# Optimization experiments

Hardware: AMD Instinct MI355X
Metric: run time of the kernel (lower is better)

Reference implementation:

```python
import jax, jax.numpy as jnp
import numpy as np

N_NODES = 50000
N_EDGES = 800000
N_GRAPHS = 512
IN_DIM, HID_DIM, EMB_DIM = 128, 256, 128
EPS = 1e-5


def setup_inputs() -> dict:
    key = jax.random.key(0)
    ks = jax.random.split(key, 12)
    x = jax.random.normal(ks[0], (N_NODES, IN_DIM), dtype=jnp.float32)
    edge_index = jax.random.randint(ks[1], (2, N_EDGES), 0, N_NODES, dtype=jnp.int32)
    batch = jnp.sort(jax.random.randint(ks[2], (N_NODES,), 0, N_GRAPHS, dtype=jnp.int32))
    s1 = 1.0 / np.sqrt(IN_DIM)
    s2 = 1.0 / np.sqrt(HID_DIM)
    return {
        "x": x,
        "edge_index": edge_index,
        "batch": batch,
        "W1": jax.random.uniform(ks[3], (IN_DIM, HID_DIM), jnp.float32, -s1, s1),
        "b1": jnp.zeros((HID_DIM,), jnp.float32),
        "gamma1": jnp.ones((HID_DIM,), jnp.float32),
        "beta1": jnp.zeros((HID_DIM,), jnp.float32),
        "W2": jax.random.uniform(ks[4], (HID_DIM, EMB_DIM), jnp.float32, -s2, s2),
        "b2": jnp.zeros((EMB_DIM,), jnp.float32),
        "gamma2": jnp.ones((EMB_DIM,), jnp.float32),
        "beta2": jnp.zeros((EMB_DIM,), jnp.float32),
    }


def _gcn_conv(x, W, b, src, dst, n_nodes):
    # PyG GCNConv: h = xW; aggregate with sym-normalized adjacency incl. self-loops; + bias
    h = x @ W  # [N, D]
    ones = jnp.ones(src.shape[0], dtype=h.dtype)
    deg = jax.ops.segment_sum(ones, dst, num_segments=n_nodes) + 1.0  # self-loop
    dinv = jax.lax.rsqrt(deg)
    norm = dinv[src] * dinv[dst]  # [E]
    msg = h[src] * norm[:, None]  # gather + scale  [E, D]
    agg = jax.ops.segment_sum(msg, dst, num_segments=n_nodes)
    agg = agg + h * (1.0 / deg)[:, None]  # self-loop contribution (norm = 1/deg)
    return agg + b


def _batchnorm(h, gamma, beta):
    mean = jnp.mean(h, axis=0)
    var = jnp.mean(jnp.square(h - mean), axis=0)  # biased, training mode
    return gamma * (h - mean) * jax.lax.rsqrt(var + EPS) + beta


def reference(x, edge_index, batch, W1, b1, gamma1, beta1, W2, b2, gamma2, beta2):
    src, dst = edge_index[0], edge_index[1]
    n = x.shape[0]
    h = _gcn_conv(x, W1, b1, src, dst, n)
    h = _batchnorm(jax.nn.relu(h), gamma1, beta1)
    h = _gcn_conv(h, W2, b2, src, dst, n)
    h = _batchnorm(jax.nn.relu(h), gamma2, beta2)
    return jax.ops.segment_max(h, batch, num_segments=N_GRAPHS)
```

## Files before the change

### kernel.cpp

```cpp
#include <hip/hip_runtime.h>
#include <math.h>

#define N_NODES 50000
#define N_EDGES 800000
#define N_GRAPHS 512
#define IN_DIM 128
#define HID_DIM 256
#define EMB_DIM 128
#define EPS 1e-5f
#define ELLW 64
#define NGROUP 8
#define GROUPN 6250
#define BLK_PER_GROUP 256
#define SCAT_BLOCKS (NGROUP * BLK_PER_GROUP)
#define NV4 (N_EDGES / 4)
#define EPV4 ((NV4 + BLK_PER_GROUP - 1) / BLK_PER_GROUP)
#define F2B_N (N_NODES * IN_DIM / 4)
#define F2B_BLOCKS ((F2B_N + 255) / 256)
#define TW1_BLOCKS ((HID_DIM * IN_DIM + 255) / 256)
#define NSLOTS 128
#define GSLOTS 128

typedef __attribute__((ext_vector_type(8))) short bf16x8;
typedef __attribute__((ext_vector_type(4))) float f32x4;
typedef __attribute__((ext_vector_type(4))) int i32x4;
typedef __attribute__((ext_vector_type(4))) unsigned short u16x4;

static __device__ __forceinline__ unsigned short f2b(float f) {
    unsigned u = __float_as_uint(f);
    return (unsigned short)((u + 0x7fffu + ((u >> 16) & 1u)) >> 16);
}
static __device__ __forceinline__ float b2f(unsigned short h) {
    return __uint_as_float(((unsigned)h) << 16);
}
static __device__ __forceinline__ float dinv_of(int d) {
    return rsqrtf((float)(min(d, ELLW) + 1));
}

__global__ void __launch_bounds__(256) scatter_convert(const int* __restrict__ src,
                                                       const int* __restrict__ dst,
                                                       int* __restrict__ fill,
                                                       int* __restrict__ col,
                                                       const float* __restrict__ x,
                                                       unsigned short* __restrict__ xbf,
                                                       const float* __restrict__ W1,
                                                       unsigned short* __restrict__ W1t) {
    int b = blockIdx.x;
    if (b < SCAT_BLOCKS) {
        int g = b & 7;
        int bs = b >> 3;
        int lo = g * GROUPN;
        int hi = lo + GROUPN;
        int i_end = min((bs + 1) * EPV4, NV4);
        const i32x4* dst4 = (const i32x4*)dst;
        const i32x4* src4 = (const i32x4*)src;
        for (int i = bs * EPV4 + threadIdx.x; i < i_end; i += 256) {
            i32x4 d4 = __builtin_nontemporal_load(&dst4[i]);
            i32x4 s4 = __builtin_nontemporal_load(&src4[i]);
#pragma unroll
            for (int e = 0; e < 4; ++e) {
                int d = d4[e];
                if (d >= lo && d < hi) {
                    int pos = min(atomicAdd(&fill[d], 1), ELLW - 1);
                    col[(d << 6) + pos] = s4[e];
                }
            }
        }
    } else if (b < SCAT_BLOCKS + F2B_BLOCKS) {
        int i = (b - SCAT_BLOCKS) * 256 + threadIdx.x;
        if (i < F2B_N) {
            f32x4 v = __builtin_nontemporal_load(&((const f32x4*)x)[i]);
            u16x4 o;
            o[0] = f2b(v[0]); o[1] = f2b(v[1]); o[2] = f2b(v[2]); o[3] = f2b(v[3]);
            __builtin_nontemporal_store(o, &((u16x4*)xbf)[i]);
        }
    } else {
        int j = (b - SCAT_BLOCKS - F2B_BLOCKS) * 256 + threadIdx.x;
        if (j < HID_DIM * IN_DIM) {
            int n = j >> 7;
            int k = j & 127;
            W1t[j] = f2b(W1[k * HID_DIM + n]);
        }
    }
}

static __device__ __forceinline__ void acc8(float* acc, uint4 r, float w) {
    const unsigned* u = (const unsigned*)&r;
#pragma unroll
    for (int k = 0; k < 4; ++k) {
        float lo = __uint_as_float((u[k] & 0xFFFFu) << 16);
        float hi = __uint_as_float(u[k] & 0xFFFF0000u);
        acc[2 * k]     += w * lo;
        acc[2 * k + 1] += w * hi;
    }
}

template <bool RELU, bool OUT_BF, bool BIAS, bool STATS>
__global__ void __launch_bounds__(256) aggw_kernel(const unsigned short* __restrict__ h,
                                                   const int* __restrict__ deg,
                                                   const int* __restrict__ col,
                                                   const float* __restrict__ bias,
                                                   void* __restrict__ y,
                                                   float* __restrict__ sumP,
                                                   float* __restrict__ sqP) {
    __shared__ float sv[STATS ? 4 : 1][STATS ? 128 : 1];
    int tid = threadIdx.x;
    int lane = tid & 63;
    int wid = tid >> 6;
    int v = blockIdx.x * 4 + wid;
    int g = lane >> 4;
    int p = lane & 15;

    int dcl = min(deg[v], ELLW);
    int cv = col[(v << 6) + lane];
    int u_l = (lane < dcl) ? cv : v;
    float w_l = (lane < dcl) ? dinv_of(deg[u_l]) : 0.f;

    uint4 selfr = make_uint4(0u, 0u, 0u, 0u);
    if (g == 0) selfr = *(const uint4*)(h + (size_t)v * 128 + p * 8);

    float acc[8] = {};
    for (int base = 0; base < dcl; base += 16) {
        int i0 = base + g, i1 = base + 4 + g, i2 = base + 8 + g, i3 = base + 12 + g;
        int u0 = __shfl(u_l, i0, 64), u1 = __shfl(u_l, i1, 64);
        int u2 = __shfl(u_l, i2, 64), u3 = __shfl(u_l, i3, 64);
        float w0 = __shfl(w_l, i0, 64), w1 = __shfl(w_l, i1, 64);
        float w2 = __shfl(w_l, i2, 64), w3 = __shfl(w_l, i3, 64);
        uint4 d0 = *(const uint4*)(h + (size_t)u0 * 128 + p * 8);
        uint4 d1 = *(const uint4*)(h + (size_t)u1 * 128 + p * 8);
        uint4 d2 = *(const uint4*)(h + (size_t)u2 * 128 + p * 8);
        uint4 d3 = *(const uint4*)(h + (size_t)u3 * 128 + p * 8);
        acc8(acc, d0, w0);
        acc8(acc, d1, w1);
        acc8(acc, d2, w2);
        acc8(acc, d3, w3);
    }

#pragma unroll
    for (int k = 0; k < 8; ++k) {
        float a = acc[k];
        a += __shfl_xor(a, 16, 64);
        a += __shfl_xor(a, 32, 64);
        acc[k] = a;
    }

    if (g == 0) {
        const unsigned* su = (const unsigned*)&selfr;
        float dv = rsqrtf((float)(dcl + 1));
        float dv2 = dv * dv;
        float o[8];
#pragma unroll
        for (int k = 0; k < 4; ++k) {
            float lo = __uint_as_float((su[k] & 0xFFFFu) << 16);
            float hi = __uint_as_float(su[k] & 0xFFFF0000u);
            o[2 * k]     = dv * acc[2 * k]     + lo * dv2;
            o[2 * k + 1] = dv * acc[2 * k + 1] + hi * dv2;
        }
        if (BIAS) {
            float4 bv0 = *(const float4*)&bias[p * 8];
            float4 bv1 = *(const float4*)&bias[p * 8 + 4];
            o[0] += bv0.x; o[1] += bv0.y; o[2] += bv0.z; o[3] += bv0.w;
            o[4] += bv1.x; o[5] += bv1.y; o[6] += bv1.z; o[7] += bv1.w;
        }
        if (RELU) {
#pragma unroll
            for (int k = 0; k < 8; ++k) o[k] = fmaxf(o[k], 0.f);
        }
        if (OUT_BF) {
            uint4 packed;
            unsigned* pu = (unsigned*)&packed;
#pragma unroll
            for (int k = 0; k < 4; ++k)
                pu[k] = (unsigned)f2b(o[2 * k]) | ((unsigned)f2b(o[2 * k + 1]) << 16);
            *(uint4*)((unsigned short*)y + (size_t)v * 128 + p * 8) = packed;
        } else {
            float* yf = (float*)y + (size_t)v * 128 + p * 8;
            *(float4*)yf = make_float4(o[0], o[1], o[2], o[3]);
            *(float4*)(yf + 4) = make_float4(o[4], o[5], o[6], o[7]);
        }
        if (STATS) {
#pragma unroll
            for (int k = 0; k < 8; ++k) sv[wid][p * 8 + k] = o[k];
        }
    }

    if (STATS) {
        __syncthreads();
        if (tid < 128) {
            float s = 0.f, q = 0.f;
#pragma unroll
            for (int w = 0; w < 4; ++w) {
                float val = sv[w][tid];
                s += val;
                q += val * val;
            }
            int slot = blockIdx.x & (NSLOTS - 1);
            atomicAdd(&sumP[slot * 128 + tid], s);
            atomicAdd(&sqP[slot * 128 + tid], q);
        }
    }
}

template <bool RELU, bool STATS>
__global__ void __launch_bounds__(256) mfma_gemm_kernel(const unsigned short* __restrict__ A,
                                                        const unsigned short* __restrict__ Bt,
                                                        const float* __restrict__ bias,
                                                        unsigned short* __restrict__ C,
                                                        float* __restrict__ sums,
                                                        float* __restrict__ sumsqs,
                                                        int M, int N, int K) {
    const int LDT = 40;
    __shared__ unsigned short As[64 * LDT];
    __shared__ unsigned short Bs[64 * LDT];
    int tid = threadIdx.x;
    int bm = blockIdx.x * 64;
    int bn = blockIdx.y * 64;
    int lr = tid >> 2;
    int lc = (tid & 3) * 8;
    int lane = tid & 63;
    int w = tid >> 6;
    int wr = (w >> 1) * 32, wc = (w & 1) * 32;
    int l15 = lane & 15, q = lane >> 4;

    f32x4 acc[2][2] = {};
    bool arow_ok = (bm + lr) < M;
    const unsigned short* Aptr = A + (size_t)(bm + lr) * K + lc;
    const unsigned short* Bptr = Bt + (size_t)(bn + lr) * K + lc;

    uint4 av = arow_ok ? *(const uint4*)(Aptr) : make_uint4(0u, 0u, 0u, 0u);
    uint4 bv = *(const uint4*)(Bptr);

    for (int k0 = 0; k0 < K; k0 += 32) {
        *(uint4*)&As[lr * LDT + lc] = av;
        *(uint4*)&Bs[lr * LDT + lc] = bv;
        __syncthreads();
        if (k0 + 32 < K) {
            av = arow_ok ? *(const uint4*)(Aptr + k0 + 32) : make_uint4(0u, 0u, 0u, 0u);
            bv = *(const uint4*)(Bptr + k0 + 32);
        }
        bf16x8 a0 = *(const bf16x8*)&As[(wr + 0 + l15) * LDT + q * 8];
        bf16x8 a1 = *(const bf16x8*)&As[(wr + 16 + l15) * LDT + q * 8];
        bf16x8 b0 = *(const bf16x8*)&Bs[(wc + 0 + l15) * LDT + q * 8];
        bf16x8 b1 = *(const bf16x8*)&Bs[(wc + 16 + l15) * LDT + q * 8];
        acc[0][0] = __builtin_amdgcn_mfma_f32_16x16x32_bf16(a0, b0, acc[0][0], 0, 0, 0);
        acc[0][1] = __builtin_amdgcn_mfma_f32_16x16x32_bf16(a0, b1, acc[0][1], 0, 0, 0);
        acc[1][0] = __builtin_amdgcn_mfma_f32_16x16x32_bf16(a1, b0, acc[1][0], 0, 0, 0);
        acc[1][1] = __builtin_amdgcn_mfma_f32_16x16x32_bf16(a1, b1, acc[1][1], 0, 0, 0);
        __syncthreads();
    }

    float scol[2] = {0.f, 0.f};
    float qcol[2] = {0.f, 0.f};
#pragma unroll
    for (int mi = 0; mi < 2; ++mi)
#pragma unroll
        for (int ni = 0; ni < 2; ++ni) {
            int colc = bn + wc + ni * 16 + l15;
            float bv2 = bias ? bias[colc] : 0.f;
#pragma unroll
            for (int r = 0; r < 4; ++r) {
                int row = bm + wr + mi * 16 + q * 4 + r;
                if (row < M) {
                    float vv = acc[mi][ni][r] + bv2;
                    if (RELU) vv = fmaxf(vv, 0.f);
                    C[(size_t)row * N + colc] = f2b(vv);
                    if (STATS) { scol[ni] += vv; qcol[ni] += vv * vv; }
                }
            }
        }

    if (STATS) {
        __shared__ float sred[4][2][16];
        __shared__ float qred[4][2][16];
#pragma unroll
        for (int ni = 0; ni < 2; ++ni) {
            float s = scol[ni], qq = qcol[ni];
            s += __shfl_xor(s, 16, 64);
            s += __shfl_xor(s, 32, 64);
            qq += __shfl_xor(qq, 16, 64);
            qq += __shfl_xor(qq, 32, 64);
            if (lane < 16) { sred[w][ni][l15] = s; qred[w][ni][l15] = qq; }
        }
        __syncthreads();
        if (tid < 64) {
            int par = (tid >> 5) & 1;
            int ni = (tid >> 4) & 1;
            int l = tid & 15;
            int slot = blockIdx.x & (GSLOTS - 1);
            atomicAdd(&sums[slot * HID_DIM + bn + tid],
                      sred[par][ni][l] + sred[par + 2][ni][l]);
            atomicAdd(&sumsqs[slot * HID_DIM + bn + tid],
                      qred[par][ni][l] + qred[par + 2][ni][l]);
        }
    }
}

__global__ void __launch_bounds__(256) prep2_kernel(const float* __restrict__ sum1P,
                                                    const float* __restrict__ sumsq1P,
                                                    const float* __restrict__ gamma1,
                                                    const float* __restrict__ beta1,
                                                    const float* __restrict__ W2,
                                                    unsigned short* __restrict__ W2pt,
                                                    float* __restrict__ bc2) {
    __shared__ float a1s[HID_DIM], s1s[HID_DIM];
    __shared__ float bp[16][17];
    int t = threadIdx.x;
    {
        float s = 0.f, q = 0.f;
#pragma unroll 8
        for (int j = 0; j < GSLOTS; ++j) {
            s += sum1P[j * HID_DIM + t];
            q += sumsq1P[j * HID_DIM + t];
        }
        float m = s * (1.f / N_NODES);
        float var = q * (1.f / N_NODES) - m * m;
        float a = gamma1[t] * rsqrtf(var + EPS);
        a1s[t] = a;
        s1s[t] = beta1[t] - m * a;
    }
    __syncthreads();
    int row = blockIdx.x * 16 + (t & 15);
    int ks = t >> 4;
    float bacc = 0.f;
    unsigned short wloc[16];
#pragma unroll
    for (int j = 0; j < 16; ++j) {
        int k = ks * 16 + j;
        float wv = W2[k * EMB_DIM + row];
        wloc[j] = f2b(a1s[k] * wv);
        bacc += s1s[k] * wv;
    }
    *(uint4*)&W2pt[(size_t)row * HID_DIM + ks * 16]     = *(uint4*)&wloc[0];
    *(uint4*)&W2pt[(size_t)row * HID_DIM + ks * 16 + 8] = *(uint4*)&wloc[8];
    bp[t & 15][ks] = bacc;
    __syncthreads();
    if (t < 16) {
        float s = 0.f;
#pragma unroll
        for (int g = 0; g < 16; ++g) s += bp[t][g];
        bc2[blockIdx.x * 16 + t] = s;
    }
}

__global__ void __launch_bounds__(128) segmax_kernel(const float* __restrict__ y,
                                                     const float* __restrict__ sumP,
                                                     const float* __restrict__ sqP,
                                                     const float* __restrict__ gamma2,
                                                     const float* __restrict__ beta2,
                                                     const int* __restrict__ batch,
                                                     float* __restrict__ out) {
    __shared__ int sh[2];
    int g = blockIdx.x;
    int c = threadIdx.x;
    float s2 = 0.f, q2 = 0.f;
#pragma unroll 8
    for (int j = 0; j < NSLOTS; ++j) {
        s2 += sumP[j * 128 + c];
        q2 += sqP[j * 128 + c];
    }
    float mch = s2 * (1.f / N_NODES);
    float var = q2 * (1.f / N_NODES) - mch * mch;
    float ac = gamma2[c] * rsqrtf(var + EPS);
    float sc = beta2[c] - mch * ac;
    if (threadIdx.x == 0) {
        int lo = 0, hi = N_NODES;
        while (lo < hi) { int mid = (lo + hi) >> 1; if (batch[mid] < g) lo = mid + 1; else hi = mid; }
        sh[0] = lo;
        hi = N_NODES;
        while (lo < hi) { int mid = (lo + hi) >> 1; if (batch[mid] < g + 1) lo = mid + 1; else hi = mid; }
        sh[1] = lo;
    }
    __syncthreads();
    int beg = sh[0], end = sh[1];
    float m = -INFINITY;
    for (int v = beg; v < end; ++v) {
        m = fmaxf(m, fmaf(ac, y[(size_t)v * EMB_DIM + c], sc));
    }
    out[(size_t)g * EMB_DIM + c] = m;
}

extern "C" void kernel_launch(void* const* d_in, const int* in_sizes, int n_in,
                              void* d_out, int out_size, void* d_ws, size_t ws_size,
                              hipStream_t stream) {
    const float* x      = (const float*)d_in[0];
    const int*   ei     = (const int*)d_in[1];
    const int*   batch  = (const int*)d_in[2];
    const float* W1     = (const float*)d_in[3];
    const float* b1     = (const float*)d_in[4];
    const float* gamma1 = (const float*)d_in[5];
    const float* beta1  = (const float*)d_in[6];
    const float* W2     = (const float*)d_in[7];
    const float* b2     = (const float*)d_in[8];
    const float* gamma2 = (const float*)d_in[9];
    const float* beta2  = (const float*)d_in[10];
    float* out = (float*)d_out;

    char* ws = (char*)d_ws;
    size_t off = 0;
    auto alloc = [&](size_t bytes) -> char* {
        char* p = ws + off;
        off = (off + bytes + 255) & ~(size_t)255;
        return p;
    };
    int*   fill    = (int*)alloc((size_t)N_NODES * 4);
    float* gsumP   = (float*)alloc((size_t)GSLOTS * HID_DIM * 4);
    float* gsqP    = (float*)alloc((size_t)GSLOTS * HID_DIM * 4);
    float* sumP    = (float*)alloc((size_t)NSLOTS * 128 * 4);
    float* sqP     = (float*)alloc((size_t)NSLOTS * 128 * 4);
    size_t zbytes = off;
    int*   col    = (int*)alloc((size_t)N_NODES * ELLW * 4);
    float* bc2    = (float*)alloc((size_t)EMB_DIM * 4);
    unsigned short* W1t  = (unsigned short*)alloc((size_t)HID_DIM * IN_DIM * 2);
    unsigned short* W2pt = (unsigned short*)alloc((size_t)HID_DIM * EMB_DIM * 2);
    unsigned short* xbf  = (unsigned short*)alloc((size_t)N_NODES * IN_DIM * 2);
    unsigned short* axbf = (unsigned short*)alloc((size_t)N_NODES * IN_DIM * 2);
    unsigned short* y1bf = (unsigned short*)alloc((size_t)N_NODES * HID_DIM * 2);
    unsigned short* gbf  = (unsigned short*)alloc((size_t)N_NODES * EMB_DIM * 2);
    float* y2 = (float*)xbf;
    (void)ws_size; (void)in_sizes; (void)n_in; (void)out_size;

    const int* src  = ei;
    const int* dstp = ei + N_EDGES;

    hipMemsetAsync(ws, 0, zbytes, stream);

    scatter_convert<<<SCAT_BLOCKS + F2B_BLOCKS + TW1_BLOCKS, 256, 0, stream>>>(
        src, dstp, fill, col, x, xbf, W1, W1t);

    aggw_kernel<false, true, false, false><<<N_NODES / 4, 256, 0, stream>>>(
        xbf, fill, col, nullptr, axbf, nullptr, nullptr);
    dim3 g1((N_NODES + 63) / 64, HID_DIM / 64);
    mfma_gemm_kernel<true, true><<<g1, 256, 0, stream>>>(axbf, W1t, b1, y1bf,
                                                         gsumP, gsqP,
                                                         N_NODES, HID_DIM, IN_DIM);

    prep2_kernel<<<8, 256, 0, stream>>>(gsumP, gsqP, gamma1, beta1, W2, W2pt, bc2);

    dim3 g2((N_NODES + 63) / 64, EMB_DIM / 64);
    mfma_gemm_kernel<false, false><<<g2, 256, 0, stream>>>(y1bf, W2pt, bc2, gbf,
                                                           nullptr, nullptr,
                                                           N_NODES, EMB_DIM, HID_DIM);
    aggw_kernel<true, false, true, true><<<N_NODES / 4, 256, 0, stream>>>(
        gbf, fill, col, b2, y2, sumP, sqP);

    segmax_kernel<<<N_GRAPHS, 128, 0, stream>>>(y2, sumP, sqP,
                                                gamma2, beta2, batch, out);
}
```

Baseline: 273.3 us.

## Build ELL adjacency via two-pass bucketed partition with shared-memory local sort

Replaces the direct global-atomic scatter into the ELL column array with a two-phase build. First, edges are partitioned into 256-node buckets using shared-memory histograms and one global atomic per bucket per block. Then a new kernel builds each bucket's ELL rows in LDS and writes them out coalesced. This trades many contended global atomics and random writes for an extra kernel launch and an intermediate buffer. It also adds a per-bucket capacity limit that would silently drop edges if a bucket overflowed.

```diff
diff --git a/kernel.cpp b/kernel.cpp
--- a/kernel.cpp
+++ b/kernel.cpp
@@ -9,12 +9,11 @@
 #define EMB_DIM 128
 #define EPS 1e-5f
 #define ELLW 64
-#define NGROUP 8
-#define GROUPN 6250
-#define BLK_PER_GROUP 256
-#define SCAT_BLOCKS (NGROUP * BLK_PER_GROUP)
 #define NV4 (N_EDGES / 4)
-#define EPV4 ((NV4 + BLK_PER_GROUP - 1) / BLK_PER_GROUP)
+#define NB 196
+#define CAP 8192
+#define PA_BLOCKS 512
+#define CPB ((NV4 + PA_BLOCKS - 1) / PA_BLOCKS)
 #define F2B_N (N_NODES * IN_DIM / 4)
 #define F2B_BLOCKS ((F2B_N + 255) / 256)
 #define TW1_BLOCKS ((HID_DIM * IN_DIM + 255) / 256)
@@ -30,44 +29,74 @@
     unsigned u = __float_as_uint(f);
     return (unsigned short)((u + 0x7fffu + ((u >> 16) & 1u)) >> 16);
 }
-static __device__ __forceinline__ float b2f(unsigned short h) {
-    return __uint_as_float(((unsigned)h) << 16);
-}
 static __device__ __forceinline__ float dinv_of(int d) {
     return rsqrtf((float)(min(d, ELLW) + 1));
 }
 
 __global__ void __launch_bounds__(256) scatter_convert(const int* __restrict__ src,
                                                        const int* __restrict__ dst,
-                                                       int* __restrict__ fill,
-                                                       int* __restrict__ col,
+                                                       int* __restrict__ gcur,
+                                                       int* __restrict__ bucketbuf,
                                                        const float* __restrict__ x,
                                                        unsigned short* __restrict__ xbf,
                                                        const float* __restrict__ W1,
                                                        unsigned short* __restrict__ W1t) {
     int b = blockIdx.x;
-    if (b < SCAT_BLOCKS) {
-        int g = b & 7;
-        int bs = b >> 3;
-        int lo = g * GROUPN;
-        int hi = lo + GROUPN;
-        int i_end = min((bs + 1) * EPV4, NV4);
+    if (b < PA_BLOCKS) {
+        __shared__ int hcnt[NB], hbase[NB], loff[NB];
+        int t = threadIdx.x;
+        for (int j = t; j < NB; j += 256) { hcnt[j] = 0; loff[j] = 0; }
+        __syncthreads();
+        int base = b * CPB;
+        int i_end = min(base + CPB, NV4);
         const i32x4* dst4 = (const i32x4*)dst;
         const i32x4* src4 = (const i32x4*)src;
-        for (int i = bs * EPV4 + threadIdx.x; i < i_end; i += 256) {
-            i32x4 d4 = __builtin_nontemporal_load(&dst4[i]);
-            i32x4 s4 = __builtin_nontemporal_load(&src4[i]);
+        int i0 = base + t, i1 = base + 256 + t;
+        bool val0 = i0 < i_end, val1 = i1 < i_end;
+        i32x4 d0 = {0, 0, 0, 0}, s0 = {0, 0, 0, 0};
+        i32x4 d1 = {0, 0, 0, 0}, s1 = {0, 0, 0, 0};
+        if (val0) {
+            d0 = __builtin_nontemporal_load(&dst4[i0]);
+            s0 = __builtin_nontemporal_load(&src4[i0]);
+        }
+        if (val1) {
+            d1 = __builtin_nontemporal_load(&dst4[i1]);
+            s1 = __builtin_nontemporal_load(&src4[i1]);
+        }
+        if (val0) {
+#pragma unroll
+            for (int e = 0; e < 4; ++e) atomicAdd(&hcnt[d0[e] >> 8], 1);
+        }
+        if (val1) {
+#pragma unroll
+            for (int e = 0; e < 4; ++e) atomicAdd(&hcnt[d1[e] >> 8], 1);
+        }
+        __syncthreads();
+        for (int j = t; j < NB; j += 256) {
+            int c = hcnt[j];
+            if (c) hbase[j] = atomicAdd(&gcur[j], c);
+        }
+        __syncthreads();
+        if (val0) {
 #pragma unroll
             for (int e = 0; e < 4; ++e) {
-                int d = d4[e];
-                if (d >= lo && d < hi) {
-                    int pos = min(atomicAdd(&fill[d], 1), ELLW - 1);
-                    col[(d << 6) + pos] = s4[e];
-                }
+                int d = d0[e], bk = d >> 8;
+                int o = atomicAdd(&loff[bk], 1);
+                int idx = hbase[bk] + o;
+                if (idx < CAP) bucketbuf[bk * CAP + idx] = ((d & 255) << 16) | s0[e];
             }
         }
-    } else if (b < SCAT_BLOCKS + F2B_BLOCKS) {
-        int i = (b - SCAT_BLOCKS) * 256 + threadIdx.x;
+        if (val1) {
+#pragma unroll
+            for (int e = 0; e < 4; ++e) {
+                int d = d1[e], bk = d >> 8;
+                int o = atomicAdd(&loff[bk], 1);
+                int idx = hbase[bk] + o;
+                if (idx < CAP) bucketbuf[bk * CAP + idx] = ((d & 255) << 16) | s1[e];
+            }
+        }
+    } else if (b < PA_BLOCKS + F2B_BLOCKS) {
+        int i = (b - PA_BLOCKS) * 256 + threadIdx.x;
         if (i < F2B_N) {
             f32x4 v = __builtin_nontemporal_load(&((const f32x4*)x)[i]);
             u16x4 o;
@@ -75,11 +104,44 @@
             __builtin_nontemporal_store(o, &((u16x4*)xbf)[i]);
         }
     } else {
-        int j = (b - SCAT_BLOCKS - F2B_BLOCKS) * 256 + threadIdx.x;
+        int j = (b - PA_BLOCKS - F2B_BLOCKS) * 256 + threadIdx.x;
         if (j < HID_DIM * IN_DIM) {
             int n = j >> 7;
             int k = j & 127;
             W1t[j] = f2b(W1[k * HID_DIM + n]);
+        }
+    }
+}
+
+__global__ void __launch_bounds__(256) build_ell(const int* __restrict__ gcur,
+                                                 const int* __restrict__ bucketbuf,
+                                                 int* __restrict__ fill,
+                                                 int* __restrict__ col) {
+    __shared__ unsigned short lcol[256 * ELLW];
+    __shared__ int lfill[256];
+    int b = blockIdx.x;
+    int t = threadIdx.x;
+    lfill[t] = 0;
+    __syncthreads();
+    int n = min(gcur[b], CAP);
+    const int* buf = bucketbuf + b * CAP;
+    for (int i = t; i < n; i += 256) {
+        int p = buf[i];
+        int dl = p >> 16;
+        int pos = atomicAdd(&lfill[dl], 1);
+        if (pos < ELLW) lcol[(dl << 6) + pos] = (unsigned short)(p & 0xFFFF);
+    }
+    __syncthreads();
+    int v = (b << 8) + t;
+    if (v < N_NODES) fill[v] = lfill[t];
+    for (int idx4 = t; idx4 < 256 * (ELLW / 4); idx4 += 256) {
+        int row = idx4 >> 4;
+        int vv = (b << 8) + row;
+        if (vv < N_NODES) {
+            int c0 = (idx4 & 15) << 2;
+            u16x4 w = *(const u16x4*)&lcol[(row << 6) + c0];
+            int4 o4 = make_int4(w[0], w[1], w[2], w[3]);
+            *(int4*)&col[((size_t)vv << 6) + c0] = o4;
         }
     }
 }
@@ -402,12 +464,14 @@
         off = (off + bytes + 255) & ~(size_t)255;
         return p;
     };
-    int*   fill    = (int*)alloc((size_t)N_NODES * 4);
+    int*   gcur    = (int*)alloc((size_t)NB * 4);
     float* gsumP   = (float*)alloc((size_t)GSLOTS * HID_DIM * 4);
     float* gsqP    = (float*)alloc((size_t)GSLOTS * HID_DIM * 4);
     float* sumP    = (float*)alloc((size_t)NSLOTS * 128 * 4);
     float* sqP     = (float*)alloc((size_t)NSLOTS * 128 * 4);
     size_t zbytes = off;
+    int*   fill   = (int*)alloc((size_t)N_NODES * 4);
+    int*   bucketbuf = (int*)alloc((size_t)NB * CAP * 4);
     int*   col    = (int*)alloc((size_t)N_NODES * ELLW * 4);
     float* bc2    = (float*)alloc((size_t)EMB_DIM * 4);
     unsigned short* W1t  = (unsigned short*)alloc((size_t)HID_DIM * IN_DIM * 2);
@@ -424,8 +488,9 @@
 
     hipMemsetAsync(ws, 0, zbytes, stream);
 
-    scatter_convert<<<SCAT_BLOCKS + F2B_BLOCKS + TW1_BLOCKS, 256, 0, stream>>>(
-        src, dstp, fill, col, x, xbf, W1, W1t);
+    scatter_convert<<<PA_BLOCKS + F2B_BLOCKS + TW1_BLOCKS, 256, 0, stream>>>(
+        src, dstp, gcur, bucketbuf, x, xbf, W1, W1t);
+    build_ell<<<NB, 256, 0, stream>>>(gcur, bucketbuf, fill, col);
 
     aggw_kernel<false, true, false, false><<<N_NODES / 4, 256, 0, stream>>>(
         xbf, fill, col, nullptr, axbf, nullptr, nullptr);
```

Result: faster. 262.4 us (-4.0%).
